# Kernel tuning notes

Measured on AMD Instinct MI355X. Metric: run time of the kernel, lower is better.

## Reference

```python
import jax, jax.numpy as jnp
import numpy as np

NUM_HEADS = 12  # per init_kwargs


def setup_inputs() -> dict:
    key = jax.random.key(0)
    k1, k2, k3 = jax.random.split(key, 3)
    B, H, W, D = 1, 64, 64, 768
    x = jax.random.normal(k1, (B, H, W, D), dtype=jnp.float32)
    # torch nn.Linear weights are [out, in]; small init keeps softmax well-conditioned
    w_qkv = jax.random.normal(k2, (3 * D, D), dtype=jnp.float32) * 0.02
    w_proj = jax.random.normal(k3, (D, D), dtype=jnp.float32) * 0.02
    b_proj = jnp.zeros((D,), dtype=jnp.float32)
    return {"x": x, "w_qkv": w_qkv, "w_proj": w_proj, "b_proj": b_proj}


def reference(x, w_qkv, w_proj, b_proj):
    B, H, W, D = x.shape
    S = H * W
    nh = NUM_HEADS
    hd = D // nh
    scale = hd ** (-0.5)
    # qkv: [B, S, 3, nh, hd] -> q,k,v each [B, nh, S, hd]
    qkv = jnp.einsum('bhwd,ed->bhwe', x, w_qkv).reshape(B, S, 3, nh, hd)
    qkv = jnp.transpose(qkv, (2, 0, 3, 1, 4))
    q, k, v = qkv[0], qkv[1], qkv[2]
    # full O(S^2) attention matrix, as in the original module
    wei = jnp.einsum('bnqd,bnkd->bnqk', q * scale, k)
    wei = jax.nn.softmax(wei, axis=-1)
    # att_drop omitted (eval mode / deterministic baseline)
    out = jnp.einsum('bnqk,bnkd->bnqd', wei, v)  # [B, nh, S, hd]
    # [B, nh, H, W, hd] -> [B, H, W, nh*hd]
    out = jnp.transpose(out.reshape(B, nh, H, W, hd), (0, 2, 3, 1, 4)).reshape(B, H, W, D)
    proj = jnp.einsum('bhwd,ed->bhwe', out, w_proj) + b_proj
    return proj
```

## Files before the change

### kernel.cpp

```cpp
#include <hip/hip_runtime.h>
#include <hip/hip_bf16.h>
#include <math.h>

typedef short s16x8 __attribute__((ext_vector_type(8)));
typedef unsigned u32x4 __attribute__((ext_vector_type(4)));
typedef float f32x4 __attribute__((ext_vector_type(4)));
typedef float f32x16 __attribute__((ext_vector_type(16)));
typedef __hip_bfloat16 bf16;

#define GLD16(g, l)                                                        \
  __builtin_amdgcn_global_load_lds(                                        \
      (const __attribute__((address_space(1))) void*)(g),                  \
      (__attribute__((address_space(3))) void*)(l), 16, 0, 0)

#define MFMA16(a, b, c) __builtin_amdgcn_mfma_f32_16x16x32_bf16((a), (b), (c), 0, 0, 0)
#define MFMA32(a, b, c) __builtin_amdgcn_mfma_f32_32x32x16_bf16((a), (b), (c), 0, 0, 0)

static constexpr int kS = 4096;
static constexpr int kD = 768;
static constexpr int kNH = 12;
static constexpr int kHD = 64;
static constexpr int kNE = 2304;

static constexpr int kNX8 = kS * kD / 8;
static constexpr int kNWq8 = kNE * kD / 8;
static constexpr int kNWp8 = kD * kD / 8;

__global__ __launch_bounds__(256)
void k_cvt3(const float* __restrict__ x, const float* __restrict__ wq,
            const float* __restrict__ wp, bf16* __restrict__ xb,
            bf16* __restrict__ wqb, bf16* __restrict__ wpb) {
  int i = blockIdx.x * 256 + threadIdx.x;
  const float* src;
  short* dst;
  if (i < kNX8) {
    src = x; dst = (short*)xb;
  } else if (i < kNX8 + kNWq8) {
    i -= kNX8; src = wq; dst = (short*)wqb;
  } else {
    i -= kNX8 + kNWq8; if (i >= kNWp8) return;
    src = wp; dst = (short*)wpb;
  }
  const f32x4 a = *(const f32x4*)(src + i * 8);
  const f32x4 b = *(const f32x4*)(src + i * 8 + 4);
  s16x8 o;
#pragma unroll
  for (int j = 0; j < 4; ++j) {
    o[j] = (short)__bfloat16_as_ushort(__float2bfloat16(a[j]));
    o[j + 4] = (short)__bfloat16_as_ushort(__float2bfloat16(b[j]));
  }
  *(s16x8*)(dst + i * 8) = o;
}

__global__ __launch_bounds__(256, 2)
void k_qkv(const bf16* __restrict__ X, const bf16* __restrict__ W,
           bf16* __restrict__ Qw, bf16* __restrict__ Kw, bf16* __restrict__ Vw) {
  __shared__ __align__(16) short As[2][128 * 32];
  __shared__ __align__(16) short Bs[2][128 * 32];
  const int tid = threadIdx.x;
  const int wv = tid >> 6, ln = tid & 63;
  const int r = ln & 15, kq = ln >> 4;
  const int bm = blockIdx.x * 128;
  const int bn = blockIdx.y * 128;
  const int wr = wv >> 1, wc = wv & 1;
  const short* Xs = (const short*)X;
  const short* Ws = (const short*)W;

  f32x4 acc[4][4] = {};

  const int c0 = wv * 128 + ln, c1 = c0 + 64;
  const int ra0 = c0 >> 2, ka0 = c0 & 3;
  const int ra1 = c1 >> 2, ka1 = c1 & 3;
  const int off0 = wv * 1024, off1 = off0 + 512;
  const short* gA0 = Xs + (bm + ra0) * kD + ka0 * 8;
  const short* gA1 = Xs + (bm + ra1) * kD + ka1 * 8;
  const short* gB0 = Ws + (bn + ra0) * kD + ka0 * 8;
  const short* gB1 = Ws + (bn + ra1) * kD + ka1 * 8;

  GLD16(gA0, &As[0][off0]);
  GLD16(gA1, &As[0][off1]);
  GLD16(gB0, &Bs[0][off0]);
  GLD16(gB1, &Bs[0][off1]);
  __syncthreads();

  const int NT = kD / 32;
  for (int t = 0; t < NT; ++t) {
    const short* aCur = As[t & 1];
    const short* bCur = Bs[t & 1];
    if (t + 1 < NT) {
      const int k1 = (t + 1) * 32;
      short* aN = As[(t + 1) & 1];
      short* bN = Bs[(t + 1) & 1];
      GLD16(gA0 + k1, aN + off0);
      GLD16(gA1 + k1, aN + off1);
      GLD16(gB0 + k1, bN + off0);
      GLD16(gB1 + k1, bN + off1);
    }
    s16x8 a[4], b[4];
#pragma unroll
    for (int i = 0; i < 4; ++i)
      a[i] = *(const s16x8*)(aCur + (wr * 64 + i * 16 + r) * 32 + kq * 8);
#pragma unroll
    for (int j = 0; j < 4; ++j)
      b[j] = *(const s16x8*)(bCur + (wc * 64 + j * 16 + r) * 32 + kq * 8);
#pragma unroll
    for (int i = 0; i < 4; ++i)
#pragma unroll
      for (int j = 0; j < 4; ++j) acc[i][j] = MFMA16(a[i], b[j], acc[i][j]);
    __syncthreads();
  }

  const int which = bn / kD;
  bf16* dst = (which == 0) ? Qw : (which == 1) ? Kw : Vw;
  const float scl = (which == 0) ? 0.125f : 1.0f;
  const int ebase = bn - which * kD + wc * 64;
#pragma unroll
  for (int j = 0; j < 4; ++j) {
    const int e = ebase + j * 16 + r;
    const int h = e >> 6, d = e & 63;
#pragma unroll
    for (int i = 0; i < 4; ++i) {
      const int srow = bm + wr * 64 + i * 16 + kq * 4;
#pragma unroll
      for (int rr = 0; rr < 4; ++rr)
        dst[(h * kS + srow + rr) * kHD + d] = __float2bfloat16(acc[i][j][rr] * scl);
    }
  }
}

__global__ __launch_bounds__(256, 2)
void k_vt(const bf16* __restrict__ Vw, bf16* __restrict__ Vt) {
  __shared__ __align__(16) short L[64 * 72];
  const int h = blockIdx.y, st = blockIdx.x;
  const int t = threadIdx.x;
  const short* src = (const short*)Vw + (h * kS + st * 64) * kHD;
  short* dstb = (short*)Vt + h * kHD * kS;
#pragma unroll
  for (int u = 0; u < 2; ++u) {
    const int c = u * 256 + t;
    const int row = c >> 3, ch = c & 7;
    *(s16x8*)(L + row * 72 + ch * 8) = *(const s16x8*)(src + row * kHD + ch * 8);
  }
  __syncthreads();
#pragma unroll
  for (int u = 0; u < 2; ++u) {
    const int c = u * 256 + t;
    const int d = c >> 3, ch = c & 7;
    s16x8 v;
#pragma unroll
    for (int j = 0; j < 8; ++j) v[j] = L[(ch * 8 + j) * 72 + d];
    *(s16x8*)(dstb + d * kS + st * 64 + ch * 8) = v;
  }
}

__global__ __launch_bounds__(256, 3)
void k_attn(const bf16* __restrict__ Qw, const bf16* __restrict__ Kw,
            const bf16* __restrict__ Vt, bf16* __restrict__ Att) {
  __shared__ __align__(16) short Ks[2][64 * 64];
  __shared__ __align__(16) short Vs[2][64 * 64];
  const int tid = threadIdx.x;
  const int wv = tid >> 6, ln = tid & 63;
  const int qh = wv >> 1;
  const int kvh = wv & 1;
  const int col = ln & 31;
  const int lh = ln >> 5;
  const int hh = blockIdx.y;
  const int q0 = blockIdx.x * 64;
  const short* Qh = (const short*)Qw + ((size_t)hh * kS + q0 + qh * 32) * kHD;
  const short* Kh = (const short*)Kw + (size_t)hh * kS * kHD;
  const short* Vh = (const short*)Vt + (size_t)hh * kHD * kS;

  s16x8 bq[4];
#pragma unroll
  for (int kb = 0; kb < 4; ++kb)
    bq[kb] = *(const s16x8*)(Qh + col * kHD + kb * 16 + lh * 8);

  f32x16 o[2] = {};
  float lp = 0.f;

  int ldso[2];
  const short* gK[2];
  const short* gV[2];
#pragma unroll
  for (int u = 0; u < 2; ++u) {
    const int c = u * 256 + tid;
    const int kr = c >> 3, g = (c & 7) ^ (kr & 7);
    ldso[u] = c * 8;
    gK[u] = Kh + kr * kHD + g * 8;
    gV[u] = Vh + kr * kS + g * 8;
  }

#pragma unroll
  for (int u = 0; u < 2; ++u) {
    GLD16(gK[u], &Ks[0][ldso[u]]);
    GLD16(gV[u], &Vs[0][ldso[u]]);
  }
  __syncthreads();

  const int NT = kS / 64;
  for (int kt = 0; kt < NT; ++kt) {
    const short* ksCur = Ks[kt & 1];
    const short* vsCur = Vs[kt & 1];
    if (kt + 1 < NT) {
      short* ksN = Ks[(kt + 1) & 1];
      short* vsN = Vs[(kt + 1) & 1];
      const int dk = (kt + 1) * 64 * kHD;
      const int dv = (kt + 1) * 64;
#pragma unroll
      for (int u = 0; u < 2; ++u) {
        GLD16(gK[u] + dk, ksN + ldso[u]);
        GLD16(gV[u] + dv, vsN + ldso[u]);
      }
    }

    f32x16 z = {};
    const int krow = kvh * 32 + col;
    const int ksw = krow & 7;
    __builtin_amdgcn_s_setprio(1);
#pragma unroll
    for (int kb = 0; kb < 4; ++kb) {
      const int ch = ((kb << 1) + lh) ^ ksw;
      s16x8 ak = *(const s16x8*)(ksCur + krow * 64 + ch * 8);
      z = MFMA32(ak, bq[kb], z);
    }
    __builtin_amdgcn_s_setprio(0);

    float p[16];
#pragma unroll
    for (int g = 0; g < 16; ++g) {
      p[g] = __expf(z[g]);
      lp += p[g];
    }
    unsigned own[8], oth[8];
#pragma unroll
    for (int m = 0; m < 4; ++m) {
      own[2 * m] = (unsigned)__bfloat16_as_ushort(__float2bfloat16(p[4 * m])) |
                   ((unsigned)__bfloat16_as_ushort(__float2bfloat16(p[4 * m + 1])) << 16);
      own[2 * m + 1] = (unsigned)__bfloat16_as_ushort(__float2bfloat16(p[4 * m + 2])) |
                       ((unsigned)__bfloat16_as_ushort(__float2bfloat16(p[4 * m + 3])) << 16);
    }
#pragma unroll
    for (int i = 0; i < 8; ++i) oth[i] = __shfl_xor(own[i], 32);

    __builtin_amdgcn_s_setprio(1);
#pragma unroll
    for (int kvk = 0; kvk < 2; ++kvk) {
      u32x4 apv;
      apv[0] = lh ? oth[4 * kvk + 2] : own[4 * kvk + 0];
      apv[1] = lh ? oth[4 * kvk + 3] : own[4 * kvk + 1];
      apv[2] = lh ? own[4 * kvk + 2] : oth[4 * kvk + 0];
      apv[3] = lh ? own[4 * kvk + 3] : oth[4 * kvk + 1];
      const s16x8 ap = __builtin_bit_cast(s16x8, apv);
      const int kvg = kvh * 2 + kvk;
#pragma unroll
      for (int db = 0; db < 2; ++db) {
        const int vrow = db * 32 + col;
        const int ch = ((kvg << 1) + lh) ^ (vrow & 7);
        s16x8 vb = *(const s16x8*)(vsCur + vrow * 64 + ch * 8);
        o[db] = MFMA32(ap, vb, o[db]);
      }
    }
    __builtin_amdgcn_s_setprio(0);
    __syncthreads();
  }

  lp += __shfl_xor(lp, 32);
  float* Of = (float*)Ks;
  float* Lf = (float*)Vs;

  if (kvh == 1) {
#pragma unroll
    for (int db = 0; db < 2; ++db)
#pragma unroll
      for (int g = 0; g < 16; ++g) {
        const int qoff = (g & 3) + 8 * (g >> 2) + 4 * lh;
        Of[(qh * 32 + qoff) * 64 + db * 32 + col] = o[db][g];
      }
    if (lh == 0) Lf[qh * 32 + col] = lp;
  }
  __syncthreads();
  if (kvh == 0) {
    lp += Lf[qh * 32 + col];
    const float inv = 1.0f / lp;
    float invq[16];
#pragma unroll
    for (int g = 0; g < 16; ++g) {
      const int qoff = (g & 3) + 8 * (g >> 2) + 4 * lh;
      invq[g] = __shfl(inv, qoff);
    }
#pragma unroll
    for (int db = 0; db < 2; ++db)
#pragma unroll
      for (int g = 0; g < 16; ++g) {
        const int qoff = (g & 3) + 8 * (g >> 2) + 4 * lh;
        const int srow = q0 + qh * 32 + qoff;
        const float val =
            (o[db][g] + Of[(qh * 32 + qoff) * 64 + db * 32 + col]) * invq[g];
        Att[srow * kD + hh * kHD + db * 32 + col] = __float2bfloat16(val);
      }
  }
}

__global__ __launch_bounds__(256, 3)
void k_proj(const bf16* __restrict__ A, const bf16* __restrict__ W,
            const float* __restrict__ Bias, float* __restrict__ Out) {
  __shared__ __align__(16) short As[2][64 * 32];
  __shared__ __align__(16) short Bs[2][64 * 32];
  const int tid = threadIdx.x;
  const int wv = tid >> 6, ln = tid & 63;
  const int r = ln & 15, kq = ln >> 4;
  const int bm = blockIdx.x * 64;
  const int bn = blockIdx.y * 64;
  const int wr = wv >> 1, wc = wv & 1;
  const short* Asrc = (const short*)A;
  const short* Wsrc = (const short*)W;

  f32x4 acc[2][2] = {};
  const int c = wv * 64 + ln;
  const int ra = c >> 2, ka = c & 3;
  const int off = wv * 512;
  const short* gA = Asrc + (bm + ra) * kD + ka * 8;
  const short* gB = Wsrc + (bn + ra) * kD + ka * 8;

  GLD16(gA, &As[0][off]);
  GLD16(gB, &Bs[0][off]);
  __syncthreads();

  const int NT = kD / 32;
  for (int t = 0; t < NT; ++t) {
    const short* aCur = As[t & 1];
    const short* bCur = Bs[t & 1];
    if (t + 1 < NT) {
      const int k1 = (t + 1) * 32;
      GLD16(gA + k1, &As[(t + 1) & 1][off]);
      GLD16(gB + k1, &Bs[(t + 1) & 1][off]);
    }
    s16x8 a[2], b[2];
#pragma unroll
    for (int i = 0; i < 2; ++i)
      a[i] = *(const s16x8*)(aCur + (wr * 32 + i * 16 + r) * 32 + kq * 8);
#pragma unroll
    for (int j = 0; j < 2; ++j)
      b[j] = *(const s16x8*)(bCur + (wc * 32 + j * 16 + r) * 32 + kq * 8);
#pragma unroll
    for (int i = 0; i < 2; ++i)
#pragma unroll
      for (int j = 0; j < 2; ++j) acc[i][j] = MFMA16(a[i], b[j], acc[i][j]);
    __syncthreads();
  }
#pragma unroll
  for (int j = 0; j < 2; ++j) {
    const int e = bn + wc * 32 + j * 16 + r;
    const float bv = Bias[e];
#pragma unroll
    for (int i = 0; i < 2; ++i) {
      const int srow = bm + wr * 32 + i * 16 + kq * 4;
#pragma unroll
      for (int rr = 0; rr < 4; ++rr)
        Out[(srow + rr) * kD + e] = acc[i][j][rr] + bv;
    }
  }
}

extern "C" void kernel_launch(void* const* d_in, const int* in_sizes, int n_in,
                              void* d_out, int out_size, void* d_ws, size_t ws_size,
                              hipStream_t stream) {
  const float* x = (const float*)d_in[0];
  const float* w_qkv = (const float*)d_in[1];
  const float* w_proj = (const float*)d_in[2];
  const float* b_proj = (const float*)d_in[3];
  float* out = (float*)d_out;

  const size_t HS = (size_t)kNH * kS * kHD;
  const int nX = kS * kD;
  const int nWq = kNE * kD;
  const int nWp = kD * kD;

  bf16* Xb = (bf16*)d_ws;
  bf16* Wqb = Xb + nX;
  bf16* Wpb = Wqb + nWq;
  bf16* Qw = Wpb + nWp;
  bf16* Kw = Qw + HS;
  bf16* Vw = Kw + HS;
  bf16* Vt = Vw + HS;
  bf16* At = Vt + HS;

  const int totalC = kNX8 + kNWq8 + kNWp8;
  k_cvt3<<<(totalC + 255) / 256, 256, 0, stream>>>(x, w_qkv, w_proj, Xb, Wqb, Wpb);

  k_qkv<<<dim3(kS / 128, kNE / 128), 256, 0, stream>>>(Xb, Wqb, Qw, Kw, Vw);
  k_vt<<<dim3(kS / 64, kNH), 256, 0, stream>>>(Vw, Vt);
  k_attn<<<dim3(kS / 64, kNH), 256, 0, stream>>>(Qw, Kw, Vt, At);
  k_proj<<<dim3(kS / 64, kD / 64), 256, 0, stream>>>(At, Wpb, b_proj, out);
}
```

Baseline: 137.6 us.

## Triple-buffer K/V tiles in attention and remap blocks for XCD-aware head locality

```diff
diff --git a/kernel.cpp b/kernel.cpp
--- a/kernel.cpp
+++ b/kernel.cpp
@@ -156,16 +156,21 @@
 __global__ __launch_bounds__(256, 3)
 void k_attn(const bf16* __restrict__ Qw, const bf16* __restrict__ Kw,
             const bf16* __restrict__ Vt, bf16* __restrict__ Att) {
-  __shared__ __align__(16) short Ks[2][64 * 64];
-  __shared__ __align__(16) short Vs[2][64 * 64];
+  __shared__ __align__(16) short Ks[3][64 * 64];
+  __shared__ __align__(16) short Vs[3][64 * 64];
   const int tid = threadIdx.x;
   const int wv = tid >> 6, ln = tid & 63;
   const int qh = wv >> 1;
   const int kvh = wv & 1;
   const int col = ln & 31;
   const int lh = ln >> 5;
-  const int hh = blockIdx.y;
-  const int q0 = blockIdx.x * 64;
+
+  const int wg = blockIdx.x;
+  const int p = (wg & 7) >> 1;
+  const int b = (((wg >> 3) << 1) | (wg & 1));
+  const int hh = 3 * p + (b >> 6);
+  const int q0 = (b & 63) * 64;
+
   const short* Qh = (const short*)Qw + ((size_t)hh * kS + q0 + qh * 32) * kHD;
   const short* Kh = (const short*)Kw + (size_t)hh * kS * kHD;
   const short* Vh = (const short*)Vt + (size_t)hh * kHD * kS;
@@ -195,17 +200,23 @@
     GLD16(gK[u], &Ks[0][ldso[u]]);
     GLD16(gV[u], &Vs[0][ldso[u]]);
   }
-  __syncthreads();
+#pragma unroll
+  for (int u = 0; u < 2; ++u) {
+    GLD16(gK[u] + 64 * kHD, &Ks[1][ldso[u]]);
+    GLD16(gV[u] + 64, &Vs[1][ldso[u]]);
+  }
+  asm volatile("s_waitcnt vmcnt(4)" ::: "memory");
+  __builtin_amdgcn_s_barrier();
 
   const int NT = kS / 64;
   for (int kt = 0; kt < NT; ++kt) {
-    const short* ksCur = Ks[kt & 1];
-    const short* vsCur = Vs[kt & 1];
-    if (kt + 1 < NT) {
-      short* ksN = Ks[(kt + 1) & 1];
-      short* vsN = Vs[(kt + 1) & 1];
-      const int dk = (kt + 1) * 64 * kHD;
-      const int dv = (kt + 1) * 64;
+    const short* ksCur = Ks[kt % 3];
+    const short* vsCur = Vs[kt % 3];
+    if (kt + 2 < NT) {
+      short* ksN = Ks[(kt + 2) % 3];
+      short* vsN = Vs[(kt + 2) % 3];
+      const int dk = (kt + 2) * 64 * kHD;
+      const int dv = (kt + 2) * 64;
 #pragma unroll
       for (int u = 0; u < 2; ++u) {
         GLD16(gK[u] + dk, ksN + ldso[u]);
@@ -225,19 +236,19 @@
     }
     __builtin_amdgcn_s_setprio(0);
 
-    float p[16];
+    float pv[16];
 #pragma unroll
     for (int g = 0; g < 16; ++g) {
-      p[g] = __expf(z[g]);
-      lp += p[g];
+      pv[g] = __expf(z[g]);
+      lp += pv[g];
     }
     unsigned own[8], oth[8];
 #pragma unroll
     for (int m = 0; m < 4; ++m) {
-      own[2 * m] = (unsigned)__bfloat16_as_ushort(__float2bfloat16(p[4 * m])) |
-                   ((unsigned)__bfloat16_as_ushort(__float2bfloat16(p[4 * m + 1])) << 16);
-      own[2 * m + 1] = (unsigned)__bfloat16_as_ushort(__float2bfloat16(p[4 * m + 2])) |
-                       ((unsigned)__bfloat16_as_ushort(__float2bfloat16(p[4 * m + 3])) << 16);
+      own[2 * m] = (unsigned)__bfloat16_as_ushort(__float2bfloat16(pv[4 * m])) |
+                   ((unsigned)__bfloat16_as_ushort(__float2bfloat16(pv[4 * m + 1])) << 16);
+      own[2 * m + 1] = (unsigned)__bfloat16_as_ushort(__float2bfloat16(pv[4 * m + 2])) |
+                       ((unsigned)__bfloat16_as_ushort(__float2bfloat16(pv[4 * m + 3])) << 16);
     }
 #pragma unroll
     for (int i = 0; i < 8; ++i) oth[i] = __shfl_xor(own[i], 32);
@@ -261,7 +272,12 @@
       }
     }
     __builtin_amdgcn_s_setprio(0);
-    __syncthreads();
+
+    if (kt + 2 < NT)
+      asm volatile("s_waitcnt vmcnt(4)" ::: "memory");
+    else
+      asm volatile("s_waitcnt vmcnt(0)" ::: "memory");
+    __builtin_amdgcn_s_barrier();
   }
 
   lp += __shfl_xor(lp, 32);
@@ -390,6 +406,6 @@
 
   k_qkv<<<dim3(kS / 128, kNE / 128), 256, 0, stream>>>(Xb, Wqb, Qw, Kw, Vw);
   k_vt<<<dim3(kS / 64, kNH), 256, 0, stream>>>(Vw, Vt);
-  k_attn<<<dim3(kS / 64, kNH), 256, 0, stream>>>(Qw, Kw, Vt, At);
+  k_attn<<<dim3((kS / 64) * kNH), 256, 0, stream>>>(Qw, Kw, Vt, At);
   k_proj<<<dim3(kS / 64, kD / 64), 256, 0, stream>>>(At, Wpb, b_proj, out);
 }
```

Result: no change. 135.7 us (-1.4%).

## Split attention KV range in two with combine kernel and permlane32 swap

Applied to the files above, without the earlier changes.

```diff
diff --git a/kernel.cpp b/kernel.cpp
--- a/kernel.cpp
+++ b/kernel.cpp
@@ -3,6 +3,7 @@
 #include <math.h>
 
 typedef short s16x8 __attribute__((ext_vector_type(8)));
+typedef unsigned u32x2 __attribute__((ext_vector_type(2)));
 typedef unsigned u32x4 __attribute__((ext_vector_type(4)));
 typedef float f32x4 __attribute__((ext_vector_type(4)));
 typedef float f32x16 __attribute__((ext_vector_type(16)));
@@ -21,6 +22,12 @@
 static constexpr int kNH = 12;
 static constexpr int kHD = 64;
 static constexpr int kNE = 2304;
+
+static __device__ __forceinline__ float bf2f(short s) {
+  union { unsigned u; float f; } x;
+  x.u = ((unsigned)(unsigned short)s) << 16;
+  return x.f;
+}
 
 static constexpr int kNX8 = kS * kD / 8;
 static constexpr int kNWq8 = kNE * kD / 8;
@@ -153,9 +160,10 @@
   }
 }
 
-__global__ __launch_bounds__(256, 3)
+__global__ __launch_bounds__(256, 5)
 void k_attn(const bf16* __restrict__ Qw, const bf16* __restrict__ Kw,
-            const bf16* __restrict__ Vt, bf16* __restrict__ Att) {
+            const bf16* __restrict__ Vt, bf16* __restrict__ Opart,
+            float* __restrict__ Lpart) {
   __shared__ __align__(16) short Ks[2][64 * 64];
   __shared__ __align__(16) short Vs[2][64 * 64];
   const int tid = threadIdx.x;
@@ -164,11 +172,20 @@
   const int kvh = wv & 1;
   const int col = ln & 31;
   const int lh = ln >> 5;
-  const int hh = blockIdx.y;
-  const int q0 = blockIdx.x * 64;
+
+  const int wg = blockIdx.x;
+  const int p = (wg & 7) >> 1;
+  const int b = ((wg >> 3) << 1) | (wg & 1);
+  const int hh = 3 * p + (b >> 7);
+  const int rem = b & 127;
+  const int qb = rem >> 1;
+  const int half = rem & 1;
+  const int q0 = qb * 64;
+  const int pidx = (hh * 64 + qb) * 2 + half;
+
   const short* Qh = (const short*)Qw + ((size_t)hh * kS + q0 + qh * 32) * kHD;
-  const short* Kh = (const short*)Kw + (size_t)hh * kS * kHD;
-  const short* Vh = (const short*)Vt + (size_t)hh * kHD * kS;
+  const short* Kh = (const short*)Kw + (size_t)hh * kS * kHD + (size_t)half * 2048 * kHD;
+  const short* Vh = (const short*)Vt + (size_t)hh * kHD * kS + half * 2048;
 
   s16x8 bq[4];
 #pragma unroll
@@ -197,11 +214,11 @@
   }
   __syncthreads();
 
-  const int NT = kS / 64;
-  for (int kt = 0; kt < NT; ++kt) {
+  const int NT2 = 32;
+  for (int kt = 0; kt < NT2; ++kt) {
     const short* ksCur = Ks[kt & 1];
     const short* vsCur = Vs[kt & 1];
-    if (kt + 1 < NT) {
+    if (kt + 1 < NT2) {
       short* ksN = Ks[(kt + 1) & 1];
       short* vsN = Vs[(kt + 1) & 1];
       const int dk = (kt + 1) * 64 * kHD;
@@ -225,31 +242,31 @@
     }
     __builtin_amdgcn_s_setprio(0);
 
-    float p[16];
+    float pv[16];
 #pragma unroll
     for (int g = 0; g < 16; ++g) {
-      p[g] = __expf(z[g]);
-      lp += p[g];
-    }
-    unsigned own[8], oth[8];
+      pv[g] = __expf(z[g]);
+      lp += pv[g];
+    }
+    unsigned own[8];
 #pragma unroll
     for (int m = 0; m < 4; ++m) {
-      own[2 * m] = (unsigned)__bfloat16_as_ushort(__float2bfloat16(p[4 * m])) |
-                   ((unsigned)__bfloat16_as_ushort(__float2bfloat16(p[4 * m + 1])) << 16);
-      own[2 * m + 1] = (unsigned)__bfloat16_as_ushort(__float2bfloat16(p[4 * m + 2])) |
-                       ((unsigned)__bfloat16_as_ushort(__float2bfloat16(p[4 * m + 3])) << 16);
-    }
-#pragma unroll
-    for (int i = 0; i < 8; ++i) oth[i] = __shfl_xor(own[i], 32);
+      own[2 * m] = (unsigned)__bfloat16_as_ushort(__float2bfloat16(pv[4 * m])) |
+                   ((unsigned)__bfloat16_as_ushort(__float2bfloat16(pv[4 * m + 1])) << 16);
+      own[2 * m + 1] = (unsigned)__bfloat16_as_ushort(__float2bfloat16(pv[4 * m + 2])) |
+                       ((unsigned)__bfloat16_as_ushort(__float2bfloat16(pv[4 * m + 3])) << 16);
+    }
 
     __builtin_amdgcn_s_setprio(1);
 #pragma unroll
     for (int kvk = 0; kvk < 2; ++kvk) {
+      u32x2 sA = __builtin_amdgcn_permlane32_swap(own[4 * kvk + 0], own[4 * kvk + 2], false, false);
+      u32x2 sB = __builtin_amdgcn_permlane32_swap(own[4 * kvk + 1], own[4 * kvk + 3], false, false);
       u32x4 apv;
-      apv[0] = lh ? oth[4 * kvk + 2] : own[4 * kvk + 0];
-      apv[1] = lh ? oth[4 * kvk + 3] : own[4 * kvk + 1];
-      apv[2] = lh ? own[4 * kvk + 2] : oth[4 * kvk + 0];
-      apv[3] = lh ? own[4 * kvk + 3] : oth[4 * kvk + 1];
+      apv[0] = sA[0];
+      apv[1] = sB[0];
+      apv[2] = sA[1];
+      apv[3] = sB[1];
       const s16x8 ap = __builtin_bit_cast(s16x8, apv);
       const int kvg = kvh * 2 + kvk;
 #pragma unroll
@@ -281,23 +298,44 @@
   __syncthreads();
   if (kvh == 0) {
     lp += Lf[qh * 32 + col];
-    const float inv = 1.0f / lp;
-    float invq[16];
-#pragma unroll
-    for (int g = 0; g < 16; ++g) {
-      const int qoff = (g & 3) + 8 * (g >> 2) + 4 * lh;
-      invq[g] = __shfl(inv, qoff);
-    }
+    if (lh == 0) Lpart[pidx * 64 + qh * 32 + col] = lp;
+    short* Ob = (short*)Opart + (size_t)pidx * 4096;
 #pragma unroll
     for (int db = 0; db < 2; ++db)
 #pragma unroll
       for (int g = 0; g < 16; ++g) {
         const int qoff = (g & 3) + 8 * (g >> 2) + 4 * lh;
-        const int srow = q0 + qh * 32 + qoff;
-        const float val =
-            (o[db][g] + Of[(qh * 32 + qoff) * 64 + db * 32 + col]) * invq[g];
-        Att[srow * kD + hh * kHD + db * 32 + col] = __float2bfloat16(val);
+        const float val = o[db][g] + Of[(qh * 32 + qoff) * 64 + db * 32 + col];
+        Ob[(qh * 32 + qoff) * 64 + db * 32 + col] =
+            (short)__bfloat16_as_ushort(__float2bfloat16(val));
       }
+  }
+}
+
+__global__ __launch_bounds__(256)
+void k_comb(const bf16* __restrict__ Opart, const float* __restrict__ Lpart,
+            bf16* __restrict__ Att) {
+  const int blk = blockIdx.x;
+  const int hh = blk >> 6, qb = blk & 63;
+  const int t = threadIdx.x;
+  const int q = t >> 2;
+  const int dg = t & 3;
+  const float inv =
+      1.0f / (Lpart[(blk * 2 + 0) * 64 + q] + Lpart[(blk * 2 + 1) * 64 + q]);
+  const short* p0 = (const short*)Opart + ((size_t)blk * 2 + 0) * 4096 + q * 64 + dg * 16;
+  const short* p1 = (const short*)Opart + ((size_t)blk * 2 + 1) * 4096 + q * 64 + dg * 16;
+  short* dst = (short*)Att + (size_t)(qb * 64 + q) * kD + hh * kHD + dg * 16;
+#pragma unroll
+  for (int j = 0; j < 2; ++j) {
+    const s16x8 a = *(const s16x8*)(p0 + j * 8);
+    const s16x8 bvv = *(const s16x8*)(p1 + j * 8);
+    s16x8 r;
+#pragma unroll
+    for (int e = 0; e < 8; ++e) {
+      const float v = (bf2f(a[e]) + bf2f(bvv[e])) * inv;
+      r[e] = (short)__bfloat16_as_ushort(__float2bfloat16(v));
+    }
+    *(s16x8*)(dst + j * 8) = r;
   }
 }
 
@@ -378,18 +416,21 @@
 
   bf16* Xb = (bf16*)d_ws;
   bf16* Wqb = Xb + nX;
-  bf16* Wpb = Wqb + nWq;
+  bf16* Vw = Wqb + nWq;
+  bf16* Wpb = Vw + HS;
   bf16* Qw = Wpb + nWp;
   bf16* Kw = Qw + HS;
-  bf16* Vw = Kw + HS;
-  bf16* Vt = Vw + HS;
+  bf16* Vt = Kw + HS;
   bf16* At = Vt + HS;
+  bf16* Opart = (bf16*)d_ws;
+  float* Lpart = (float*)((short*)d_ws + (size_t)1536 * 4096);
 
   const int totalC = kNX8 + kNWq8 + kNWp8;
   k_cvt3<<<(totalC + 255) / 256, 256, 0, stream>>>(x, w_qkv, w_proj, Xb, Wqb, Wpb);
 
   k_qkv<<<dim3(kS / 128, kNE / 128), 256, 0, stream>>>(Xb, Wqb, Qw, Kw, Vw);
   k_vt<<<dim3(kS / 64, kNH), 256, 0, stream>>>(Vw, Vt);
-  k_attn<<<dim3(kS / 64, kNH), 256, 0, stream>>>(Qw, Kw, Vt, At);
+  k_attn<<<dim3(2 * (kS / 64) * kNH), 256, 0, stream>>>(Qw, Kw, Vt, Opart, Lpart);
+  k_comb<<<dim3((kS / 64) * kNH), 256, 0, stream>>>(Opart, Lpart, At);
   k_proj<<<dim3(kS / 64, kD / 64), 256, 0, stream>>>(At, Wpb, b_proj, out);
 }
```

New measurement: 133.0 us. -3.3%, faster.
